# Kernel optimization log

Hardware: AMD Instinct MI355X
Metric: run time of the kernel (lower is better)

Reference implementation:

```python
import jax, jax.numpy as jnp
import numpy as np

DIM = 512
HEADS = 8
DIM_HEAD = 64
INNER = HEADS * DIM_HEAD  # 512
SCALE = DIM_HEAD ** -0.5


def layer_norm(x, w, b, eps=1e-5):
    mu = jnp.mean(x, axis=-1, keepdims=True)
    var = jnp.var(x, axis=-1, keepdims=True)
    return (x - mu) * jax.lax.rsqrt(var + eps) * w + b


def setup_inputs() -> dict:
    key = jax.random.key(0)
    ks = jax.random.split(key, 8)
    b, n = 8, 1024
    img = jax.random.normal(ks[0], (b, n, DIM), dtype=jnp.float32)
    tab = jax.random.normal(ks[1], (b, 1, DIM), dtype=jnp.float32)
    # params (fan-in scaled)
    w_qkv = jax.random.normal(ks[2], (DIM, 3 * INNER), dtype=jnp.float32) / np.sqrt(DIM)
    w_tab_qkv = jax.random.normal(ks[3], (DIM, 3 * INNER), dtype=jnp.float32) / np.sqrt(DIM)
    w_out = jax.random.normal(ks[4], (INNER, DIM), dtype=jnp.float32) / np.sqrt(INNER)
    b_out = jax.random.normal(ks[5], (DIM,), dtype=jnp.float32) * 0.01
    ln_w = jnp.ones((DIM,), dtype=jnp.float32)
    ln_b = jnp.zeros((DIM,), dtype=jnp.float32)
    return {"img": img, "tab": tab, "w_qkv": w_qkv, "w_tab_qkv": w_tab_qkv,
            "w_out": w_out, "b_out": b_out, "ln_w": ln_w, "ln_b": ln_b}


def reference(img, tab, w_qkv, w_tab_qkv, w_out, b_out, ln_w, ln_b):
    b, n, _ = img.shape
    x = layer_norm(img, ln_w, ln_b)
    qkv = x @ w_qkv  # [b, n, 3*inner]
    q, k, v = jnp.split(qkv, 3, axis=-1)

    def to_heads(t, s):
        return t.reshape(b, s, HEADS, DIM_HEAD).transpose(0, 2, 1, 3)  # [b,h,s,d]

    q, k, v = to_heads(q, n), to_heads(k, n), to_heads(v, n)

    t = layer_norm(tab, ln_w, ln_b)
    qkv_t = t @ w_tab_qkv  # [b, 1, 3*inner]
    _, k_t, v_t = jnp.split(qkv_t, 3, axis=-1)
    k = jnp.concatenate([k, to_heads(k_t, 1)], axis=2)  # [b,h,n+1,d]
    v = jnp.concatenate([v, to_heads(v_t, 1)], axis=2)

    dots = jnp.einsum('bhqd,bhkd->bhqk', q, k) * SCALE  # [b,h,n,n+1]
    attn = jax.nn.softmax(dots, axis=-1)
    out = jnp.einsum('bhqk,bhkd->bhqd', attn, v)
    out = out.transpose(0, 2, 1, 3).reshape(b, n, INNER)
    return out @ w_out + b_out
```

## Files before the change

kernel.cpp:

```cpp
#include <hip/hip_runtime.h>


typedef __attribute__((ext_vector_type(4))) float f32x4;
typedef __attribute__((ext_vector_type(16))) float f32x16;
typedef __attribute__((ext_vector_type(8))) short bf16x8;
typedef __attribute__((ext_vector_type(8))) unsigned short u16x8;

#define MFMA16(a, b, c) __builtin_amdgcn_mfma_f32_16x16x32_bf16(a, b, c, 0, 0, 0)
#define MFMA32(a, b, c) __builtin_amdgcn_mfma_f32_32x32x16_bf16(a, b, c, 0, 0, 0)

#define GLD16(gsrc, ldst)                                                     \
  __builtin_amdgcn_global_load_lds(                                           \
      (const __attribute__((address_space(1))) void*)(gsrc),                  \
      (__attribute__((address_space(3))) void*)(ldst), 16, 0, 0)

#define KPAD 1088

#define QSCALE 0.18033688011112042f

__device__ __forceinline__ unsigned short f2bf(float f) {
  union { float f; unsigned int u; } c; c.f = f;
  unsigned int u = c.u;
  u += 0x7fffu + ((u >> 16) & 1u);
  return (unsigned short)(u >> 16);
}

__device__ __forceinline__ unsigned int cvtpk_bf16(float lo, float hi) {
  unsigned int r;
  asm("v_cvt_pk_bf16_f32 %0, %1, %2" : "=v"(r) : "v"(lo), "v"(hi));
  return r;
}

__global__ __launch_bounds__(256) void k_prep(const float* __restrict__ w_qkv,
                                              const float* __restrict__ w_out,
                                              unsigned short* __restrict__ wqt,
                                              unsigned short* __restrict__ wot) {
  __shared__ unsigned short t[64][68];
  int blk = blockIdx.x, tid = threadIdx.x;
  const float* src;
  unsigned short* dst;
  int k0, n0, ldin;
  if (blk < 192) {
    int ti = blk / 24, tj = blk % 24;
    k0 = ti * 64; n0 = tj * 64; ldin = 1536;
    src = w_qkv; dst = wqt;
  } else {
    int g = blk - 192;
    int ti = g >> 3, tj = g & 7;
    k0 = ti * 64; n0 = tj * 64; ldin = 512;
    src = w_out; dst = wot;
  }
  int rr = tid >> 4, c4 = (tid & 15) * 4;
  #pragma unroll
  for (int i = 0; i < 4; ++i) {
    int r = i * 16 + rr;
    float4 v = *(const float4*)(src + (size_t)(k0 + r) * ldin + n0 + c4);
    t[c4 + 0][r] = f2bf(v.x);
    t[c4 + 1][r] = f2bf(v.y);
    t[c4 + 2][r] = f2bf(v.z);
    t[c4 + 3][r] = f2bf(v.w);
  }
  __syncthreads();
  #pragma unroll
  for (int i = 0; i < 4; ++i) {
    int r = i * 16 + rr;
    ushort4 w = *(const ushort4*)&t[r][c4];
    *(ushort4*)(dst + (size_t)(n0 + r) * 512 + k0 + c4) = w;
  }
}

__global__ __launch_bounds__(256) void k_ln(const float* __restrict__ img,
                                            const float* __restrict__ tab,
                                            const float* __restrict__ ln_w,
                                            const float* __restrict__ ln_b,
                                            unsigned short* __restrict__ x_bf,
                                            float* __restrict__ t_ln) {
  int wid = threadIdx.x >> 6, lane = threadIdx.x & 63;
  int row = blockIdx.x * 4 + wid;
  if (row >= 8200) return;
  const float* src = (row < 8192) ? img + (size_t)row * 512
                                  : tab + (size_t)(row - 8192) * 512;
  float4 v0 = *(const float4*)(src + lane * 8);
  float4 v1 = *(const float4*)(src + lane * 8 + 4);
  float x[8] = {v0.x, v0.y, v0.z, v0.w, v1.x, v1.y, v1.z, v1.w};
  float s = 0.f, sq = 0.f;
  #pragma unroll
  for (int j = 0; j < 8; ++j) { s += x[j]; sq += x[j] * x[j]; }
  #pragma unroll
  for (int off = 32; off >= 1; off >>= 1) {
    s  += __shfl_xor(s, off);
    sq += __shfl_xor(sq, off);
  }
  float mean = s * (1.0f / 512.0f);
  float var  = sq * (1.0f / 512.0f) - mean * mean;
  float rs = rsqrtf(var + 1e-5f);
  float4 w0 = *(const float4*)(ln_w + lane * 8);
  float4 w1 = *(const float4*)(ln_w + lane * 8 + 4);
  float4 b0 = *(const float4*)(ln_b + lane * 8);
  float4 b1 = *(const float4*)(ln_b + lane * 8 + 4);
  float w[8] = {w0.x, w0.y, w0.z, w0.w, w1.x, w1.y, w1.z, w1.w};
  float bb[8] = {b0.x, b0.y, b0.z, b0.w, b1.x, b1.y, b1.z, b1.w};
  float y[8];
  #pragma unroll
  for (int j = 0; j < 8; ++j) y[j] = (x[j] - mean) * rs * w[j] + bb[j];
  if (row < 8192) {
    bf16x8 o;
    #pragma unroll
    for (int j = 0; j < 8; ++j) o[j] = (short)f2bf(y[j]);
    *(bf16x8*)(x_bf + (size_t)row * 512 + lane * 8) = o;
  } else {
    float* dst = t_ln + (size_t)(row - 8192) * 512 + lane * 8;
    *(float4*)dst       = make_float4(y[0], y[1], y[2], y[3]);
    *(float4*)(dst + 4) = make_float4(y[4], y[5], y[6], y[7]);
  }
}

__global__ __launch_bounds__(256) void k_tab(const float* __restrict__ t_ln,
                                             const float* __restrict__ w_tab,
                                             unsigned short* __restrict__ kh,
                                             unsigned short* __restrict__ vt) {
  __shared__ float red[4][64];
  int blk = blockIdx.x;
  int b = blk >> 4, chunk = blk & 15;
  int t = threadIdx.x;
  int cl = t & 63;
  int ks = t >> 6;
  int col = chunk * 64 + cl;

  {
    int h = chunk & 7;
    int bh = b * 8 + h;
    u16x8 z = (u16x8)(0);
    if (chunk < 8) {
      unsigned short* base = kh + ((size_t)bh * KPAD + 1024) * 64;
      #pragma unroll
      for (int i = 0; i < 2; ++i)
        *(u16x8*)(base + (t + i * 256) * 8) = z;
    } else {
      #pragma unroll
      for (int i = 0; i < 2; ++i) {
        int idx = t + i * 256;
        int d = idx >> 3, ch = idx & 7;
        *(u16x8*)(vt + ((size_t)bh * 64 + d) * KPAD + 1024 + ch * 8) = z;
      }
    }
  }

  const float* tl = t_ln + b * 512;
  const float* wp = w_tab + 512 + col + (size_t)(ks * 128) * 1536;
  float s = 0.f;
  #pragma unroll 8
  for (int k = 0; k < 128; ++k)
    s += tl[ks * 128 + k] * wp[(size_t)k * 1536];
  red[ks][cl] = s;
  __syncthreads();
  if (ks == 0) {
    float v = red[0][cl] + red[1][cl] + red[2][cl] + red[3][cl];
    int part = col >> 9, hd = col & 511, h = hd >> 6, d = hd & 63;
    int bh = b * 8 + h;
    unsigned short hv = f2bf(v);
    if (part == 0) kh[((size_t)bh * KPAD + 1024) * 64 + d] = hv;
    else           vt[((size_t)bh * 64 + d) * KPAD + 1024] = hv;
  }
}

__global__ __launch_bounds__(256) void k_qkv(const unsigned short* __restrict__ x_bf,
                                             const unsigned short* __restrict__ wqt,
                                             unsigned short* __restrict__ qh,
                                             unsigned short* __restrict__ kh,
                                             unsigned short* __restrict__ vt) {
  __shared__ unsigned short As[2][128 * 32];
  __shared__ unsigned short Bs[2][128 * 32];
  int tid = threadIdx.x;
  int wid = tid >> 6, lane = tid & 63;
  int bm = blockIdx.x & 63, bn = blockIdx.x >> 6;
  int r0 = bm * 128, c0 = bn * 128;
  int lr = lane & 15, lk = (lane >> 4) * 8;
  int wr = (wid >> 1) * 64, wc = (wid & 1) * 64;
  int srow = lane >> 2, scol = (lane & 3) * 8;
  const unsigned short* gA0 = x_bf + (size_t)(r0 + (wid * 2 + 0) * 16 + srow) * 512 + scol;
  const unsigned short* gA1 = x_bf + (size_t)(r0 + (wid * 2 + 1) * 16 + srow) * 512 + scol;
  const unsigned short* gB0 = wqt  + (size_t)(c0 + (wid * 2 + 0) * 16 + srow) * 512 + scol;
  const unsigned short* gB1 = wqt  + (size_t)(c0 + (wid * 2 + 1) * 16 + srow) * 512 + scol;
  int o0 = (wid * 2 + 0) * 512, o1 = (wid * 2 + 1) * 512;

  f32x4 acc[4][4];
  #pragma unroll
  for (int mi = 0; mi < 4; ++mi)
    #pragma unroll
    for (int ni = 0; ni < 4; ++ni)
      acc[mi][ni] = (f32x4){0.f, 0.f, 0.f, 0.f};

  GLD16(gA0, &As[0][o0]);
  GLD16(gA1, &As[0][o1]);
  GLD16(gB0, &Bs[0][o0]);
  GLD16(gB1, &Bs[0][o1]);
  GLD16(gA0 + 32, &As[1][o0]);
  GLD16(gA1 + 32, &As[1][o1]);
  GLD16(gB0 + 32, &Bs[1][o0]);
  GLD16(gB1 + 32, &Bs[1][o1]);

  int cur = 0;
  for (int t = 0; t < 16; ++t) {
    if (t < 15) asm volatile("s_waitcnt vmcnt(4)" ::: "memory");
    else        asm volatile("s_waitcnt vmcnt(0)" ::: "memory");
    __builtin_amdgcn_s_barrier();
    bf16x8 af[4], bfr[4];
    #pragma unroll
    for (int mi = 0; mi < 4; ++mi)
      af[mi] = *(const bf16x8*)&As[cur][(wr + mi * 16 + lr) * 32 + lk];
    #pragma unroll
    for (int ni = 0; ni < 4; ++ni)
      bfr[ni] = *(const bf16x8*)&Bs[cur][(wc + ni * 16 + lr) * 32 + lk];
    __builtin_amdgcn_s_setprio(1);
    #pragma unroll
    for (int mi = 0; mi < 4; ++mi)
      #pragma unroll
      for (int ni = 0; ni < 4; ++ni)
        acc[mi][ni] = MFMA16(af[mi], bfr[ni], acc[mi][ni]);
    __builtin_amdgcn_s_setprio(0);
    __builtin_amdgcn_s_barrier();
    asm volatile("" ::: "memory");
    if (t < 14) {
      int k2 = (t + 2) * 32;
      GLD16(gA0 + k2, &As[cur][o0]);
      GLD16(gA1 + k2, &As[cur][o1]);
      GLD16(gB0 + k2, &Bs[cur][o0]);
      GLD16(gB1 + k2, &Bs[cur][o1]);
    }
    cur ^= 1;
  }

  #pragma unroll
  for (int ni = 0; ni < 4; ++ni) {
    int col0 = c0 + wc + ni * 16;
    int which = col0 >> 9;
    int hh = (col0 & 511) >> 6;
    int d = (col0 & 63) + lr;
    #pragma unroll
    for (int mi = 0; mi < 4; ++mi)
      #pragma unroll
      for (int reg = 0; reg < 4; ++reg) {
        int row = r0 + wr + mi * 16 + (lane >> 4) * 4 + reg;
        int b = row >> 10, n = row & 1023;
        int bh = b * 8 + hh;
        float v = acc[mi][ni][reg];
        if (which == 0) {
          qh[((size_t)bh * 1024 + n) * 64 + d] = f2bf(v * QSCALE);
        } else if (which == 1) {
          kh[((size_t)bh * KPAD + n) * 64 + d] = f2bf(v);
        } else {
          vt[((size_t)bh * 64 + d) * KPAD + n] = f2bf(v);
        }
      }
  }
}

__global__ __launch_bounds__(512, 4) void k_attn(const unsigned short* __restrict__ qh,
                                                 const unsigned short* __restrict__ kh,
                                                 const unsigned short* __restrict__ vt,
                                                 unsigned short* __restrict__ ao) {
  __shared__ __align__(16) unsigned short Ks[2][4096];
  __shared__ __align__(16) unsigned short Vs[2][4096];
  int tid = threadIdx.x;
  int wid = tid >> 6, lane = tid & 63;
  int bid = blockIdx.x;
  int swz = ((bid & 7) << 5) | (bid >> 3);
  int bh = swz >> 2;
  int q0 = (swz & 3) * 256 + wid * 32;
  int lq = lane & 31, half = lane >> 5;

  const unsigned short* Q  = qh + (size_t)bh * 1024 * 64;
  const unsigned short* Kg = kh + (size_t)bh * KPAD * 64;
  const unsigned short* Vg = vt + (size_t)bh * 64 * KPAD;

  int xr = tid >> 3;
  int xc = (tid & 7) ^ (xr & 7);
  const unsigned short* kg_src = Kg + xr * 64 + xc * 8;
  const unsigned short* vg_src = Vg + (size_t)xr * KPAD + xc * 8;
  unsigned short* kdstA = &Ks[0][wid * 512];
  unsigned short* kdstB = &Ks[1][wid * 512];
  unsigned short* vdstA = &Vs[0][wid * 512];
  unsigned short* vdstB = &Vs[1][wid * 512];

  bf16x8 qf[4];
  const unsigned short* qlane = Q + (size_t)(q0 + lq) * 64 + half * 8;
  #pragma unroll
  for (int dt = 0; dt < 4; ++dt)
    qf[dt] = *(const bf16x8*)(qlane + dt * 16);

  f32x16 o0 = (f32x16)(0.0f), o1 = (f32x16)(0.0f);
  float m = -1e30f, lsum = 0.f;

  GLD16(kg_src, kdstA);
  GLD16(vg_src, vdstA);
  __syncthreads();

  for (int kt = 0; kt < 17; ++kt) {
    int cur = kt & 1;
    if (kt < 16) {
      GLD16(kg_src + (kt + 1) * 4096, cur ? kdstA : kdstB);
      GLD16(vg_src + (kt + 1) * 64,   cur ? vdstA : vdstB);
    }
    const unsigned short* Kb = Ks[cur];
    const unsigned short* Vb = Vs[cur];
    #pragma unroll
    for (int sub = 0; sub < 2; ++sub) {
      int krow = sub * 32 + lq;
      bf16x8 kf[4];
      #pragma unroll
      for (int dt = 0; dt < 4; ++dt) {
        int ch = (half + dt * 2) ^ (krow & 7);
        kf[dt] = *(const bf16x8*)&Kb[krow * 64 + ch * 8];
      }
      f32x16 s = (f32x16)(0.0f);
      __builtin_amdgcn_s_setprio(1);
      #pragma unroll
      for (int dt = 0; dt < 4; ++dt)
        s = MFMA32(kf[dt], qf[dt], s);
      __builtin_amdgcn_s_setprio(0);
      if (kt == 16) {
        if (sub == 0) {
          #pragma unroll
          for (int reg = 0; reg < 16; ++reg) {
            if (reg == 0) { if (half) s[0] = -1e30f; }
            else s[reg] = -1e30f;
          }
        } else {
          #pragma unroll
          for (int reg = 0; reg < 16; ++reg) s[reg] = -1e30f;
        }
      }
      float pmax = s[0];
      #pragma unroll
      for (int reg = 1; reg < 16; ++reg) pmax = fmaxf(pmax, s[reg]);
      pmax = fmaxf(pmax, __shfl_xor(pmax, 32));
      if (!__all(pmax <= m + 8.0f)) {
        float mnew = fmaxf(m, pmax);
        float al = __builtin_amdgcn_exp2f(m - mnew);
        lsum *= al;
        #pragma unroll
        for (int reg = 0; reg < 16; ++reg) { o0[reg] *= al; o1[reg] *= al; }
        m = mnew;
      }
      float p[16];
      float ls = 0.f;
      #pragma unroll
      for (int reg = 0; reg < 16; ++reg) {
        p[reg] = __builtin_amdgcn_exp2f(s[reg] - m);
        ls += p[reg];
      }
      lsum += ls;
      unsigned int c0x0 = cvtpk_bf16(p[0],  p[1]);
      unsigned int c0x1 = cvtpk_bf16(p[2],  p[3]);
      unsigned int c0y0 = cvtpk_bf16(p[4],  p[5]);
      unsigned int c0y1 = cvtpk_bf16(p[6],  p[7]);
      unsigned int c1x0 = cvtpk_bf16(p[8],  p[9]);
      unsigned int c1x1 = cvtpk_bf16(p[10], p[11]);
      unsigned int c1y0 = cvtpk_bf16(p[12], p[13]);
      unsigned int c1y1 = cvtpk_bf16(p[14], p[15]);
      asm volatile("v_permlane32_swap_b32 %0, %1" : "+v"(c0x0), "+v"(c0y0));
      asm volatile("v_permlane32_swap_b32 %0, %1" : "+v"(c0x1), "+v"(c0y1));
      asm volatile("v_permlane32_swap_b32 %0, %1" : "+v"(c1x0), "+v"(c1y0));
      asm volatile("v_permlane32_swap_b32 %0, %1" : "+v"(c1x1), "+v"(c1y1));
      union { unsigned int w[4]; bf16x8 v; } f0, f1;
      f0.w[0] = c0x0; f0.w[1] = c0x1; f0.w[2] = c0y0; f0.w[3] = c0y1;
      f1.w[0] = c1x0; f1.w[1] = c1x1; f1.w[2] = c1y0; f1.w[3] = c1y1;
      int vr0 = lq, vr1 = lq + 32;
      int cb = sub * 4 + half;
      bf16x8 vf0 = *(const bf16x8*)&Vb[vr0 * 64 + ((cb + 0) ^ (vr0 & 7)) * 8];
      bf16x8 vf1 = *(const bf16x8*)&Vb[vr0 * 64 + ((cb + 2) ^ (vr0 & 7)) * 8];
      bf16x8 vf2 = *(const bf16x8*)&Vb[vr1 * 64 + ((cb + 0) ^ (vr1 & 7)) * 8];
      bf16x8 vf3 = *(const bf16x8*)&Vb[vr1 * 64 + ((cb + 2) ^ (vr1 & 7)) * 8];
      __builtin_amdgcn_s_setprio(1);
      o0 = MFMA32(vf0, f0.v, o0);
      o0 = MFMA32(vf1, f1.v, o0);
      o1 = MFMA32(vf2, f0.v, o1);
      o1 = MFMA32(vf3, f1.v, o1);
      __builtin_amdgcn_s_setprio(0);
    }
    __syncthreads();
  }
  lsum += __shfl_xor(lsum, 32);
  float rl = 1.0f / lsum;
  int b = bh >> 3, h = bh & 7;
  unsigned short* aorow = ao + ((size_t)(b * 1024 + q0 + lq)) * 512 + h * 64;
  #pragma unroll
  for (int dt2 = 0; dt2 < 2; ++dt2) {
    #pragma unroll
    for (int g = 0; g < 4; ++g) {
      ushort4 pk;
      float v0 = (dt2 ? o1[4 * g + 0] : o0[4 * g + 0]) * rl;
      float v1 = (dt2 ? o1[4 * g + 1] : o0[4 * g + 1]) * rl;
      float v2 = (dt2 ? o1[4 * g + 2] : o0[4 * g + 2]) * rl;
      float v3 = (dt2 ? o1[4 * g + 3] : o0[4 * g + 3]) * rl;
      pk.x = f2bf(v0); pk.y = f2bf(v1); pk.z = f2bf(v2); pk.w = f2bf(v3);
      *(ushort4*)(aorow + dt2 * 32 + 8 * g + 4 * half) = pk;
    }
  }
}

__global__ __launch_bounds__(256) void k_out(const unsigned short* __restrict__ ao,
                                             const unsigned short* __restrict__ wot,
                                             const float* __restrict__ b_out,
                                             float* __restrict__ out) {
  __shared__ unsigned short As[2][128 * 32];
  __shared__ unsigned short Bs[2][128 * 32];
  int tid = threadIdx.x;
  int wid = tid >> 6, lane = tid & 63;
  int bm = blockIdx.x & 63, bn = blockIdx.x >> 6;
  int r0 = bm * 128, c0 = bn * 128;
  int lr = lane & 15, lk = (lane >> 4) * 8;
  int wr = (wid >> 1) * 64, wc = (wid & 1) * 64;
  int srow = lane >> 2, scol = (lane & 3) * 8;
  const unsigned short* gA0 = ao  + (size_t)(r0 + (wid * 2 + 0) * 16 + srow) * 512 + scol;
  const unsigned short* gA1 = ao  + (size_t)(r0 + (wid * 2 + 1) * 16 + srow) * 512 + scol;
  const unsigned short* gB0 = wot + (size_t)(c0 + (wid * 2 + 0) * 16 + srow) * 512 + scol;
  const unsigned short* gB1 = wot + (size_t)(c0 + (wid * 2 + 1) * 16 + srow) * 512 + scol;
  int o0 = (wid * 2 + 0) * 512, o1 = (wid * 2 + 1) * 512;

  f32x4 acc[4][4];
  #pragma unroll
  for (int mi = 0; mi < 4; ++mi)
    #pragma unroll
    for (int ni = 0; ni < 4; ++ni)
      acc[mi][ni] = (f32x4){0.f, 0.f, 0.f, 0.f};

  GLD16(gA0, &As[0][o0]);
  GLD16(gA1, &As[0][o1]);
  GLD16(gB0, &Bs[0][o0]);
  GLD16(gB1, &Bs[0][o1]);
  GLD16(gA0 + 32, &As[1][o0]);
  GLD16(gA1 + 32, &As[1][o1]);
  GLD16(gB0 + 32, &Bs[1][o0]);
  GLD16(gB1 + 32, &Bs[1][o1]);

  int cur = 0;
  for (int t = 0; t < 16; ++t) {
    if (t < 15) asm volatile("s_waitcnt vmcnt(4)" ::: "memory");
    else        asm volatile("s_waitcnt vmcnt(0)" ::: "memory");
    __builtin_amdgcn_s_barrier();
    bf16x8 af[4], bfr[4];
    #pragma unroll
    for (int mi = 0; mi < 4; ++mi)
      af[mi] = *(const bf16x8*)&As[cur][(wr + mi * 16 + lr) * 32 + lk];
    #pragma unroll
    for (int ni = 0; ni < 4; ++ni)
      bfr[ni] = *(const bf16x8*)&Bs[cur][(wc + ni * 16 + lr) * 32 + lk];
    __builtin_amdgcn_s_setprio(1);
    #pragma unroll
    for (int mi = 0; mi < 4; ++mi)
      #pragma unroll
      for (int ni = 0; ni < 4; ++ni)
        acc[mi][ni] = MFMA16(af[mi], bfr[ni], acc[mi][ni]);
    __builtin_amdgcn_s_setprio(0);
    __builtin_amdgcn_s_barrier();
    asm volatile("" ::: "memory");
    if (t < 14) {
      int k2 = (t + 2) * 32;
      GLD16(gA0 + k2, &As[cur][o0]);
      GLD16(gA1 + k2, &As[cur][o1]);
      GLD16(gB0 + k2, &Bs[cur][o0]);
      GLD16(gB1 + k2, &Bs[cur][o1]);
    }
    cur ^= 1;
  }

  #pragma unroll
  for (int ni = 0; ni < 4; ++ni) {
    int col = c0 + wc + ni * 16 + lr;
    float bias = b_out[col];
    #pragma unroll
    for (int mi = 0; mi < 4; ++mi)
      #pragma unroll
      for (int reg = 0; reg < 4; ++reg) {
        int row = r0 + wr + mi * 16 + (lane >> 4) * 4 + reg;
        out[(size_t)row * 512 + col] = acc[mi][ni][reg] + bias;
      }
  }
}

extern "C" void kernel_launch(void* const* d_in, const int* in_sizes, int n_in,
                              void* d_out, int out_size, void* d_ws, size_t ws_size,
                              hipStream_t stream) {
  const float* img       = (const float*)d_in[0];
  const float* tab       = (const float*)d_in[1];
  const float* w_qkv     = (const float*)d_in[2];
  const float* w_tab_qkv = (const float*)d_in[3];
  const float* w_out     = (const float*)d_in[4];
  const float* b_out     = (const float*)d_in[5];
  const float* ln_w      = (const float*)d_in[6];
  const float* ln_b      = (const float*)d_in[7];
  char* ws = (char*)d_ws;
  unsigned short* x_bf = (unsigned short*)(ws);
  unsigned short* wqt  = (unsigned short*)(ws + 8388608);
  unsigned short* wot  = (unsigned short*)(ws + 9961472);
  unsigned short* qh   = (unsigned short*)(ws + 10485760);
  unsigned short* kh   = (unsigned short*)(ws + 18874368);
  unsigned short* vt   = (unsigned short*)(ws + 27787264);
  unsigned short* ao   = (unsigned short*)(ws + 36700160);
  float*          t_ln = (float*)(ws + 45088768);
  float* out = (float*)d_out;

  hipLaunchKernelGGL(k_prep, dim3(256),  dim3(256), 0, stream, w_qkv, w_out, wqt, wot);
  hipLaunchKernelGGL(k_ln,   dim3(2050), dim3(256), 0, stream, img, tab, ln_w, ln_b, x_bf, t_ln);
  hipLaunchKernelGGL(k_tab,  dim3(128),  dim3(256), 0, stream, t_ln, w_tab_qkv, kh, vt);
  hipLaunchKernelGGL(k_qkv,  dim3(768),  dim3(256), 0, stream, x_bf, wqt, qh, kh, vt);
  hipLaunchKernelGGL(k_attn, dim3(256),  dim3(512), 0, stream, qh, kh, vt, ao);
  hipLaunchKernelGGL(k_out,  dim3(256),  dim3(256), 0, stream, ao, wot, b_out, out);
}
```

Baseline: 88.72 us.

## Merge prep, layernorm and tab kernels; triple-buffer GEMM prefetch with one barrier

Three preprocessing kernels (weight transpose/cast, row layernorm, tab KV projection) are combined into one launch that dispatches on block index. The tab blocks now compute their own layernorm in shared memory, so the t_ln workspace round trip and two launch gaps go away. The QKV and output GEMMs move from a two-stage to a three-stage LDS ring. Each k-step now issues its prefetch right after the first barrier and drops the second barrier. This costs more LDS per block, which may reduce occupancy.

Result: faster. 82.76 us (-6.7%).

```diff
diff --git a/kernel.cpp b/kernel.cpp
--- a/kernel.cpp
+++ b/kernel.cpp
@@ -31,136 +31,144 @@
   return r;
 }
 
-__global__ __launch_bounds__(256) void k_prep(const float* __restrict__ w_qkv,
-                                              const float* __restrict__ w_out,
-                                              unsigned short* __restrict__ wqt,
-                                              unsigned short* __restrict__ wot) {
-  __shared__ unsigned short t[64][68];
+__global__ __launch_bounds__(256) void k_pre(const float* __restrict__ img,
+                                             const float* __restrict__ tab,
+                                             const float* __restrict__ w_qkv,
+                                             const float* __restrict__ w_tab,
+                                             const float* __restrict__ w_out,
+                                             const float* __restrict__ ln_w,
+                                             const float* __restrict__ ln_b,
+                                             unsigned short* __restrict__ x_bf,
+                                             unsigned short* __restrict__ wqt,
+                                             unsigned short* __restrict__ wot,
+                                             unsigned short* __restrict__ kh,
+                                             unsigned short* __restrict__ vt) {
   int blk = blockIdx.x, tid = threadIdx.x;
-  const float* src;
-  unsigned short* dst;
-  int k0, n0, ldin;
-  if (blk < 192) {
-    int ti = blk / 24, tj = blk % 24;
-    k0 = ti * 64; n0 = tj * 64; ldin = 1536;
-    src = w_qkv; dst = wqt;
-  } else {
-    int g = blk - 192;
-    int ti = g >> 3, tj = g & 7;
-    k0 = ti * 64; n0 = tj * 64; ldin = 512;
-    src = w_out; dst = wot;
-  }
-  int rr = tid >> 4, c4 = (tid & 15) * 4;
-  #pragma unroll
-  for (int i = 0; i < 4; ++i) {
-    int r = i * 16 + rr;
-    float4 v = *(const float4*)(src + (size_t)(k0 + r) * ldin + n0 + c4);
-    t[c4 + 0][r] = f2bf(v.x);
-    t[c4 + 1][r] = f2bf(v.y);
-    t[c4 + 2][r] = f2bf(v.z);
-    t[c4 + 3][r] = f2bf(v.w);
-  }
-  __syncthreads();
-  #pragma unroll
-  for (int i = 0; i < 4; ++i) {
-    int r = i * 16 + rr;
-    ushort4 w = *(const ushort4*)&t[r][c4];
-    *(ushort4*)(dst + (size_t)(n0 + r) * 512 + k0 + c4) = w;
-  }
-}
-
-__global__ __launch_bounds__(256) void k_ln(const float* __restrict__ img,
-                                            const float* __restrict__ tab,
-                                            const float* __restrict__ ln_w,
-                                            const float* __restrict__ ln_b,
-                                            unsigned short* __restrict__ x_bf,
-                                            float* __restrict__ t_ln) {
-  int wid = threadIdx.x >> 6, lane = threadIdx.x & 63;
-  int row = blockIdx.x * 4 + wid;
-  if (row >= 8200) return;
-  const float* src = (row < 8192) ? img + (size_t)row * 512
-                                  : tab + (size_t)(row - 8192) * 512;
-  float4 v0 = *(const float4*)(src + lane * 8);
-  float4 v1 = *(const float4*)(src + lane * 8 + 4);
-  float x[8] = {v0.x, v0.y, v0.z, v0.w, v1.x, v1.y, v1.z, v1.w};
-  float s = 0.f, sq = 0.f;
-  #pragma unroll
-  for (int j = 0; j < 8; ++j) { s += x[j]; sq += x[j] * x[j]; }
-  #pragma unroll
-  for (int off = 32; off >= 1; off >>= 1) {
-    s  += __shfl_xor(s, off);
-    sq += __shfl_xor(sq, off);
-  }
-  float mean = s * (1.0f / 512.0f);
-  float var  = sq * (1.0f / 512.0f) - mean * mean;
-  float rs = rsqrtf(var + 1e-5f);
-  float4 w0 = *(const float4*)(ln_w + lane * 8);
-  float4 w1 = *(const float4*)(ln_w + lane * 8 + 4);
-  float4 b0 = *(const float4*)(ln_b + lane * 8);
-  float4 b1 = *(const float4*)(ln_b + lane * 8 + 4);
-  float w[8] = {w0.x, w0.y, w0.z, w0.w, w1.x, w1.y, w1.z, w1.w};
-  float bb[8] = {b0.x, b0.y, b0.z, b0.w, b1.x, b1.y, b1.z, b1.w};
-  float y[8];
-  #pragma unroll
-  for (int j = 0; j < 8; ++j) y[j] = (x[j] - mean) * rs * w[j] + bb[j];
-  if (row < 8192) {
+  if (blk < 256) {
+    __shared__ unsigned short tbuf[64][68];
+    const float* src;
+    unsigned short* dst;
+    int k0, n0, ldin;
+    if (blk < 192) {
+      int ti = blk / 24, tj = blk % 24;
+      k0 = ti * 64; n0 = tj * 64; ldin = 1536;
+      src = w_qkv; dst = wqt;
+    } else {
+      int g = blk - 192;
+      int ti = g >> 3, tj = g & 7;
+      k0 = ti * 64; n0 = tj * 64; ldin = 512;
+      src = w_out; dst = wot;
+    }
+    int rr = tid >> 4, c4 = (tid & 15) * 4;
+    #pragma unroll
+    for (int i = 0; i < 4; ++i) {
+      int r = i * 16 + rr;
+      float4 v = *(const float4*)(src + (size_t)(k0 + r) * ldin + n0 + c4);
+      tbuf[c4 + 0][r] = f2bf(v.x);
+      tbuf[c4 + 1][r] = f2bf(v.y);
+      tbuf[c4 + 2][r] = f2bf(v.z);
+      tbuf[c4 + 3][r] = f2bf(v.w);
+    }
+    __syncthreads();
+    #pragma unroll
+    for (int i = 0; i < 4; ++i) {
+      int r = i * 16 + rr;
+      ushort4 w = *(const ushort4*)&tbuf[r][c4];
+      *(ushort4*)(dst + (size_t)(n0 + r) * 512 + k0 + c4) = w;
+    }
+  } else if (blk < 2304) {
+    int wid = tid >> 6, lane = tid & 63;
+    int row = (blk - 256) * 4 + wid;
+    const float* src = img + (size_t)row * 512;
+    float4 v0 = *(const float4*)(src + lane * 8);
+    float4 v1 = *(const float4*)(src + lane * 8 + 4);
+    float x[8] = {v0.x, v0.y, v0.z, v0.w, v1.x, v1.y, v1.z, v1.w};
+    float s = 0.f, sq = 0.f;
+    #pragma unroll
+    for (int j = 0; j < 8; ++j) { s += x[j]; sq += x[j] * x[j]; }
+    #pragma unroll
+    for (int off = 32; off >= 1; off >>= 1) {
+      s  += __shfl_xor(s, off);
+      sq += __shfl_xor(sq, off);
+    }
+    float mean = s * (1.0f / 512.0f);
+    float var  = sq * (1.0f / 512.0f) - mean * mean;
+    float rs = rsqrtf(var + 1e-5f);
+    float4 w0 = *(const float4*)(ln_w + lane * 8);
+    float4 w1 = *(const float4*)(ln_w + lane * 8 + 4);
+    float4 b0 = *(const float4*)(ln_b + lane * 8);
+    float4 b1 = *(const float4*)(ln_b + lane * 8 + 4);
+    float w[8] = {w0.x, w0.y, w0.z, w0.w, w1.x, w1.y, w1.z, w1.w};
+    float bb[8] = {b0.x, b0.y, b0.z, b0.w, b1.x, b1.y, b1.z, b1.w};
     bf16x8 o;
     #pragma unroll
-    for (int j = 0; j < 8; ++j) o[j] = (short)f2bf(y[j]);
+    for (int j = 0; j < 8; ++j)
+      o[j] = (short)f2bf((x[j] - mean) * rs * w[j] + bb[j]);
     *(bf16x8*)(x_bf + (size_t)row * 512 + lane * 8) = o;
   } else {
-    float* dst = t_ln + (size_t)(row - 8192) * 512 + lane * 8;
-    *(float4*)dst       = make_float4(y[0], y[1], y[2], y[3]);
-    *(float4*)(dst + 4) = make_float4(y[4], y[5], y[6], y[7]);
-  }
-}
-
-__global__ __launch_bounds__(256) void k_tab(const float* __restrict__ t_ln,
-                                             const float* __restrict__ w_tab,
-                                             unsigned short* __restrict__ kh,
-                                             unsigned short* __restrict__ vt) {
-  __shared__ float red[4][64];
-  int blk = blockIdx.x;
-  int b = blk >> 4, chunk = blk & 15;
-  int t = threadIdx.x;
-  int cl = t & 63;
-  int ks = t >> 6;
-  int col = chunk * 64 + cl;
-
-  {
-    int h = chunk & 7;
-    int bh = b * 8 + h;
-    u16x8 z = (u16x8)(0);
-    if (chunk < 8) {
-      unsigned short* base = kh + ((size_t)bh * KPAD + 1024) * 64;
-      #pragma unroll
-      for (int i = 0; i < 2; ++i)
-        *(u16x8*)(base + (t + i * 256) * 8) = z;
-    } else {
-      #pragma unroll
-      for (int i = 0; i < 2; ++i) {
-        int idx = t + i * 256;
-        int d = idx >> 3, ch = idx & 7;
-        *(u16x8*)(vt + ((size_t)bh * 64 + d) * KPAD + 1024 + ch * 8) = z;
-      }
-    }
-  }
-
-  const float* tl = t_ln + b * 512;
-  const float* wp = w_tab + 512 + col + (size_t)(ks * 128) * 1536;
-  float s = 0.f;
-  #pragma unroll 8
-  for (int k = 0; k < 128; ++k)
-    s += tl[ks * 128 + k] * wp[(size_t)k * 1536];
-  red[ks][cl] = s;
-  __syncthreads();
-  if (ks == 0) {
-    float v = red[0][cl] + red[1][cl] + red[2][cl] + red[3][cl];
-    int part = col >> 9, hd = col & 511, h = hd >> 6, d = hd & 63;
-    int bh = b * 8 + h;
-    unsigned short hv = f2bf(v);
-    if (part == 0) kh[((size_t)bh * KPAD + 1024) * 64 + d] = hv;
-    else           vt[((size_t)bh * 64 + d) * KPAD + 1024] = hv;
+    __shared__ float tl[512];
+    __shared__ float red[4][64];
+    __shared__ float ws_[4], wq_[4];
+    int blk2 = blk - 2304;
+    int b = blk2 >> 4, chunk = blk2 & 15;
+    int t = tid;
+    int lane = t & 63, wid = t >> 6;
+    int cl = t & 63;
+    int ks = t >> 6;
+    int col = chunk * 64 + cl;
+
+    {
+      int h = chunk & 7;
+      int bh = b * 8 + h;
+      u16x8 z = (u16x8)(0);
+      if (chunk < 8) {
+        unsigned short* base = kh + ((size_t)bh * KPAD + 1024) * 64;
+        #pragma unroll
+        for (int i = 0; i < 2; ++i)
+          *(u16x8*)(base + (t + i * 256) * 8) = z;
+      } else {
+        #pragma unroll
+        for (int i = 0; i < 2; ++i) {
+          int idx = t + i * 256;
+          int d = idx >> 3, ch = idx & 7;
+          *(u16x8*)(vt + ((size_t)bh * 64 + d) * KPAD + 1024 + ch * 8) = z;
+        }
+      }
+    }
+
+    float2 tv = *(const float2*)(tab + (size_t)b * 512 + t * 2);
+    float s_ = tv.x + tv.y, q_ = tv.x * tv.x + tv.y * tv.y;
+    #pragma unroll
+    for (int off = 32; off >= 1; off >>= 1) {
+      s_ += __shfl_xor(s_, off);
+      q_ += __shfl_xor(q_, off);
+    }
+    if (lane == 0) { ws_[wid] = s_; wq_[wid] = q_; }
+    __syncthreads();
+    float S = ws_[0] + ws_[1] + ws_[2] + ws_[3];
+    float Qq = wq_[0] + wq_[1] + wq_[2] + wq_[3];
+    float mean = S * (1.0f / 512.0f);
+    float var = Qq * (1.0f / 512.0f) - mean * mean;
+    float rs = rsqrtf(var + 1e-5f);
+    tl[t * 2 + 0] = (tv.x - mean) * rs * ln_w[t * 2 + 0] + ln_b[t * 2 + 0];
+    tl[t * 2 + 1] = (tv.y - mean) * rs * ln_w[t * 2 + 1] + ln_b[t * 2 + 1];
+    __syncthreads();
+
+    const float* wp = w_tab + 512 + col + (size_t)(ks * 128) * 1536;
+    float s = 0.f;
+    #pragma unroll 8
+    for (int k = 0; k < 128; ++k)
+      s += tl[ks * 128 + k] * wp[(size_t)k * 1536];
+    red[ks][cl] = s;
+    __syncthreads();
+    if (ks == 0) {
+      float v = red[0][cl] + red[1][cl] + red[2][cl] + red[3][cl];
+      int part = col >> 9, hd = col & 511, h = hd >> 6, d = hd & 63;
+      int bh = b * 8 + h;
+      unsigned short hv = f2bf(v);
+      if (part == 0) kh[((size_t)bh * KPAD + 1024) * 64 + d] = hv;
+      else           vt[((size_t)bh * 64 + d) * KPAD + 1024] = hv;
+    }
   }
 }
 
@@ -169,8 +177,8 @@
                                              unsigned short* __restrict__ qh,
                                              unsigned short* __restrict__ kh,
                                              unsigned short* __restrict__ vt) {
-  __shared__ unsigned short As[2][128 * 32];
-  __shared__ unsigned short Bs[2][128 * 32];
+  __shared__ unsigned short As[3][128 * 32];
+  __shared__ unsigned short Bs[3][128 * 32];
   int tid = threadIdx.x;
   int wid = tid >> 6, lane = tid & 63;
   int bm = blockIdx.x & 63, bn = blockIdx.x >> 6;
@@ -200,11 +208,18 @@
   GLD16(gB0 + 32, &Bs[1][o0]);
   GLD16(gB1 + 32, &Bs[1][o1]);
 
-  int cur = 0;
+  int cur = 0, pre = 2;
   for (int t = 0; t < 16; ++t) {
     if (t < 15) asm volatile("s_waitcnt vmcnt(4)" ::: "memory");
     else        asm volatile("s_waitcnt vmcnt(0)" ::: "memory");
     __builtin_amdgcn_s_barrier();
+    if (t < 14) {
+      int k2 = (t + 2) * 32;
+      GLD16(gA0 + k2, &As[pre][o0]);
+      GLD16(gA1 + k2, &As[pre][o1]);
+      GLD16(gB0 + k2, &Bs[pre][o0]);
+      GLD16(gB1 + k2, &Bs[pre][o1]);
+    }
     bf16x8 af[4], bfr[4];
     #pragma unroll
     for (int mi = 0; mi < 4; ++mi)
@@ -219,16 +234,8 @@
       for (int ni = 0; ni < 4; ++ni)
         acc[mi][ni] = MFMA16(af[mi], bfr[ni], acc[mi][ni]);
     __builtin_amdgcn_s_setprio(0);
-    __builtin_amdgcn_s_barrier();
-    asm volatile("" ::: "memory");
-    if (t < 14) {
-      int k2 = (t + 2) * 32;
-      GLD16(gA0 + k2, &As[cur][o0]);
-      GLD16(gA1 + k2, &As[cur][o1]);
-      GLD16(gB0 + k2, &Bs[cur][o0]);
-      GLD16(gB1 + k2, &Bs[cur][o1]);
-    }
-    cur ^= 1;
+    cur = (cur == 2) ? 0 : cur + 1;
+    pre = (pre == 2) ? 0 : pre + 1;
   }
 
   #pragma unroll
@@ -404,8 +411,8 @@
                                              const unsigned short* __restrict__ wot,
                                              const float* __restrict__ b_out,
                                              float* __restrict__ out) {
-  __shared__ unsigned short As[2][128 * 32];
-  __shared__ unsigned short Bs[2][128 * 32];
+  __shared__ unsigned short As[3][128 * 32];
+  __shared__ unsigned short Bs[3][128 * 32];
   int tid = threadIdx.x;
   int wid = tid >> 6, lane = tid & 63;
   int bm = blockIdx.x & 63, bn = blockIdx.x >> 6;
@@ -435,11 +442,18 @@
   GLD16(gB0 + 32, &Bs[1][o0]);
   GLD16(gB1 + 32, &Bs[1][o1]);
 
-  int cur = 0;
+  int cur = 0, pre = 2;
   for (int t = 0; t < 16; ++t) {
     if (t < 15) asm volatile("s_waitcnt vmcnt(4)" ::: "memory");
     else        asm volatile("s_waitcnt vmcnt(0)" ::: "memory");
     __builtin_amdgcn_s_barrier();
+    if (t < 14) {
+      int k2 = (t + 2) * 32;
+      GLD16(gA0 + k2, &As[pre][o0]);
+      GLD16(gA1 + k2, &As[pre][o1]);
+      GLD16(gB0 + k2, &Bs[pre][o0]);
+      GLD16(gB1 + k2, &Bs[pre][o1]);
+    }
     bf16x8 af[4], bfr[4];
     #pragma unroll
     for (int mi = 0; mi < 4; ++mi)
@@ -454,16 +468,8 @@
       for (int ni = 0; ni < 4; ++ni)
         acc[mi][ni] = MFMA16(af[mi], bfr[ni], acc[mi][ni]);
     __builtin_amdgcn_s_setprio(0);
-    __builtin_amdgcn_s_barrier();
-    asm volatile("" ::: "memory");
-    if (t < 14) {
-      int k2 = (t + 2) * 32;
-      GLD16(gA0 + k2, &As[cur][o0]);
-      GLD16(gA1 + k2, &As[cur][o1]);
-      GLD16(gB0 + k2, &Bs[cur][o0]);
-      GLD16(gB1 + k2, &Bs[cur][o1]);
-    }
-    cur ^= 1;
+    cur = (cur == 2) ? 0 : cur + 1;
+    pre = (pre == 2) ? 0 : pre + 1;
   }
 
   #pragma unroll
@@ -499,12 +505,11 @@
   unsigned short* kh   = (unsigned short*)(ws + 18874368);
   unsigned short* vt   = (unsigned short*)(ws + 27787264);
   unsigned short* ao   = (unsigned short*)(ws + 36700160);
-  float*          t_ln = (float*)(ws + 45088768);
   float* out = (float*)d_out;
 
-  hipLaunchKernelGGL(k_prep, dim3(256),  dim3(256), 0, stream, w_qkv, w_out, wqt, wot);
-  hipLaunchKernelGGL(k_ln,   dim3(2050), dim3(256), 0, stream, img, tab, ln_w, ln_b, x_bf, t_ln);
-  hipLaunchKernelGGL(k_tab,  dim3(128),  dim3(256), 0, stream, t_ln, w_tab_qkv, kh, vt);
+  hipLaunchKernelGGL(k_pre,  dim3(2432), dim3(256), 0, stream,
+                     img, tab, w_qkv, w_tab_qkv, w_out, ln_w, ln_b,
+                     x_bf, wqt, wot, kh, vt);
   hipLaunchKernelGGL(k_qkv,  dim3(768),  dim3(256), 0, stream, x_bf, wqt, qh, kh, vt);
   hipLaunchKernelGGL(k_attn, dim3(256),  dim3(512), 0, stream, qh, kh, vt, ao);
   hipLaunchKernelGGL(k_out,  dim3(256),  dim3(256), 0, stream, ao, wot, b_out, out);
```
